# Optimization experiments

Hardware: AMD Instinct MI355X
Metric: run time of the kernel (lower is better)

## Reference

```python
import jax, jax.numpy as jnp
import numpy as np

B, N = 512, 500  # batch (cells), n_nodes (genes)


def setup_inputs() -> dict:
    key = jax.random.key(0)
    k1, k2, k3, k4 = jax.random.split(key, 4)
    x = jax.random.normal(k1, (B, N), dtype=jnp.float32)
    # GumbelAdjacency edge logits (bicycle initializes these near a constant; random here)
    log_alpha = jax.random.normal(k2, (N, N), dtype=jnp.float32)
    # single Linear(n_nodes, n_nodes, bias=False) weight, torch layout [out, in]
    W = jax.random.normal(k3, (N, N), dtype=jnp.float32) / np.sqrt(N).astype(np.float32)
    # uniform noise consumed by the gumbel-sigmoid sampler (one draw per batch element)
    u = jax.random.uniform(k4, (B, N, N), dtype=jnp.float32)
    return {"x": x, "log_alpha": log_alpha, "W": W, "u": u}


def reference(x, log_alpha, W, u):
    # --- GumbelAdjacency.forward(num_batch): hard gumbel-sigmoid sample, tau=1 ---
    eps = 1e-6
    uc = jnp.clip(u, eps, 1.0 - eps)
    logistic = jnp.log(uc) - jnp.log(1.0 - uc)            # logistic(0,1) noise
    y_soft = jax.nn.sigmoid(log_alpha[None, :, :] + logistic)  # [B, N, N]
    y_hard = (y_soft > 0.5).astype(y_soft.dtype)
    adj = y_soft + jax.lax.stop_gradient(y_hard - y_soft)  # straight-through

    # --- per-node masked MLP loop, fused ---
    # original: f_x[b, i] = tanh( (mask_i * adj[b, :, i] * x[b]) @ W.T )[i]
    #                     = tanh( sum_{j != i} W[i, j] * adj[b, j, i] * x[b, j] )
    mask = 1.0 - jnp.eye(N, dtype=x.dtype)                # mask[j, i] = 0 iff j == i
    gated = adj * mask[None, :, :]                        # [B, j, i]
    f_x = jnp.tanh(jnp.einsum('bji,bj,ij->bi', gated, x, W))  # [B, N]
    return f_x
```

## Files before the change

kernel.cpp:

```cpp
#include <hip/hip_runtime.h>
#include <math.h>

#define NN 500
#define BB 512
#define NCHUNK 4
#define JCH (NN / NCHUNK)

__device__ __forceinline__ bool np_decision(float laf, float v) {
    float l1 = (float)log((double)v);
    float s  = 1.0f - v;
    float l2 = (float)log((double)s);
    float logistic = l1 - l2;
    float z  = laf + logistic;
    float e  = (float)exp(-(double)z);
    float d  = 1.0f + e;
    float y  = 1.0f / d;
    return y > 0.5f;
}

__global__ void prep_kernel(const float* __restrict__ la,
                            const float* __restrict__ W,
                            float2* __restrict__ WU) {
    int idx = blockIdx.x * blockDim.x + threadIdx.x;
    if (idx >= NN * NN) return;
    int j = idx / NN;
    int i = idx - j * NN;
    float laf = la[idx];

    const float LO = 1e-6f;
    const float HI = (float)(1.0 - 1e-6);

    float U;
    if (!np_decision(laf, HI)) {
        U = __builtin_inff();
    } else if (np_decision(laf, LO)) {
        U = 0.0f;
    } else {
        unsigned lo = __float_as_uint(LO);
        unsigned hi = __float_as_uint(HI);
        double T  = 1.0 / (1.0 + exp((double)laf));
        float  Tf = fminf(fmaxf((float)T, LO), HI);
        unsigned g = __float_as_uint(Tf);
        unsigned a = (g > lo + 1024u) ? g - 1024u : lo;
        unsigned b = (g + 1024u < hi) ? g + 1024u : hi;
        if (!np_decision(laf, __uint_as_float(b))) {
            lo = b;
        } else {
            hi = b;
            if (np_decision(laf, __uint_as_float(a))) hi = a; else lo = a;
        }
        while (hi - lo > 1u) {
            unsigned mid = lo + (hi - lo) / 2u;
            if (np_decision(laf, __uint_as_float(mid))) hi = mid; else lo = mid;
        }
        U = __uint_as_float(hi);
    }
    float w = (i == j) ? 0.0f : W[i * NN + j];
    WU[idx] = make_float2(w, U);
}

__global__ __launch_bounds__(256) void fused_kernel(
        const float* __restrict__ x,
        const float* __restrict__ u,
        const float4* __restrict__ WU4,
        float* __restrict__ P) {
    __shared__ float xs[JCH];
    const int bid = blockIdx.x;
    const int b = bid >> 2;
    const int c = bid & 3;
    const int j0 = c * JCH;
    const int t = threadIdx.x;
    if (t < JCH) xs[t] = x[b * NN + j0 + t];
    __syncthreads();
    if (t >= NN / 2) return;

    const float2* __restrict__ u2 = (const float2*)(u + (size_t)b * NN * NN) + j0 * (NN / 2);
    const float4* __restrict__ wu = WU4 + j0 * (NN / 2);

    const float LO = 1e-6f;
    const float HI = (float)(1.0 - 1e-6);

    float acc0 = 0.0f, acc1 = 0.0f;
#pragma unroll 5
    for (int j = 0; j < JCH; ++j) {
        const int k = j * (NN / 2) + t;
        float2 uv = u2[k];
        float4 wv = wu[k];
        float  xj = xs[j];
        float uc0 = fminf(fmaxf(uv.x, LO), HI);
        float uc1 = fminf(fmaxf(uv.y, LO), HI);
        if (uc0 >= wv.y) acc0 += wv.x * xj;
        if (uc1 >= wv.w) acc1 += wv.z * xj;
    }
    float2 o = make_float2(acc0, acc1);
    ((float2*)(P + (size_t)c * BB * NN + b * NN))[t] = o;
}

__global__ __launch_bounds__(256) void reduce_kernel(const float* __restrict__ P,
                                                     float* __restrict__ out) {
    int n = blockIdx.x * blockDim.x + threadIdx.x;
    if (n >= BB * NN) return;
    const int S = BB * NN;
    float s = P[n] + P[S + n] + P[2 * S + n] + P[3 * S + n];
    out[n] = tanhf(s);
}

extern "C" void kernel_launch(void* const* d_in, const int* in_sizes, int n_in,
                              void* d_out, int out_size, void* d_ws, size_t ws_size,
                              hipStream_t stream) {
    const float* x  = (const float*)d_in[0];
    const float* la = (const float*)d_in[1];
    const float* W  = (const float*)d_in[2];
    const float* u  = (const float*)d_in[3];
    float* out = (float*)d_out;

    float2* WU = (float2*)d_ws;
    float*  P  = (float*)((char*)d_ws + (size_t)NN * NN * sizeof(float2));

    int prep_blocks = (NN * NN + 255) / 256;
    prep_kernel<<<prep_blocks, 256, 0, stream>>>(la, W, WU);
    fused_kernel<<<BB * NCHUNK, 256, 0, stream>>>(x, u, (const float4*)WU, P);
    reduce_kernel<<<(BB * NN + 255) / 256, 256, 0, stream>>>(P, out);
}
```

Before: 707.8 us.

## Share WU loads across four batch rows and use nontemporal u loads

The fused kernel now handles four batch elements per block, so each loaded WU entry (weight and threshold) serves four u rows instead of one. It also splits the j dimension into 10 chunks instead of 4, loads u with nontemporal hints, and drops the redundant clamp of u. The reduce kernel is vectorised to float4 and sums 10 partials, which makes the partial buffer larger. The prep bisection now starts with a narrower ±32-ulp bracket around the guess.

```diff
diff --git a/kernel.cpp b/kernel.cpp
--- a/kernel.cpp
+++ b/kernel.cpp
@@ -3,8 +3,12 @@
 
 #define NN 500
 #define BB 512
-#define NCHUNK 4
+#define BGRP 4
+#define NCHUNK 10
 #define JCH (NN / NCHUNK)
+#define NPAIR (NN / 2)
+
+using f2 = __attribute__((ext_vector_type(2))) float;
 
 __device__ __forceinline__ bool np_decision(float laf, float v) {
     float l1 = (float)log((double)v);
@@ -41,13 +45,13 @@
         double T  = 1.0 / (1.0 + exp((double)laf));
         float  Tf = fminf(fmaxf((float)T, LO), HI);
         unsigned g = __float_as_uint(Tf);
-        unsigned a = (g > lo + 1024u) ? g - 1024u : lo;
-        unsigned b = (g + 1024u < hi) ? g + 1024u : hi;
-        if (!np_decision(laf, __uint_as_float(b))) {
-            lo = b;
-        } else {
-            hi = b;
+        unsigned a = (g > lo + 32u) ? g - 32u : lo;
+        unsigned b = (g + 32u < hi) ? g + 32u : hi;
+        if (a > lo) {
             if (np_decision(laf, __uint_as_float(a))) hi = a; else lo = a;
+        }
+        if (b > lo && b < hi) {
+            if (np_decision(laf, __uint_as_float(b))) hi = b; else lo = b;
         }
         while (hi - lo > 1u) {
             unsigned mid = lo + (hi - lo) / 2u;
@@ -64,45 +68,65 @@
         const float* __restrict__ u,
         const float4* __restrict__ WU4,
         float* __restrict__ P) {
-    __shared__ float xs[JCH];
+    __shared__ float xs[BGRP][JCH];
     const int bid = blockIdx.x;
-    const int b = bid >> 2;
-    const int c = bid & 3;
+    const int bg = bid / NCHUNK;
+    const int c  = bid - bg * NCHUNK;
+    const int b0 = bg * BGRP;
     const int j0 = c * JCH;
     const int t = threadIdx.x;
-    if (t < JCH) xs[t] = x[b * NN + j0 + t];
+    if (t < BGRP * JCH) {
+        int bl = t / JCH;
+        int j  = t - bl * JCH;
+        xs[bl][j] = x[(b0 + bl) * NN + j0 + j];
+    }
     __syncthreads();
-    if (t >= NN / 2) return;
+    if (t >= NPAIR) return;
 
-    const float2* __restrict__ u2 = (const float2*)(u + (size_t)b * NN * NN) + j0 * (NN / 2);
-    const float4* __restrict__ wu = WU4 + j0 * (NN / 2);
+    const f2* __restrict__ u0 = (const f2*)(u + (size_t)(b0 + 0) * NN * NN);
+    const f2* __restrict__ u1 = (const f2*)(u + (size_t)(b0 + 1) * NN * NN);
+    const f2* __restrict__ u2 = (const f2*)(u + (size_t)(b0 + 2) * NN * NN);
+    const f2* __restrict__ u3 = (const f2*)(u + (size_t)(b0 + 3) * NN * NN);
 
-    const float LO = 1e-6f;
-    const float HI = (float)(1.0 - 1e-6);
-
-    float acc0 = 0.0f, acc1 = 0.0f;
+    float a00 = 0.0f, a01 = 0.0f, a10 = 0.0f, a11 = 0.0f;
+    float a20 = 0.0f, a21 = 0.0f, a30 = 0.0f, a31 = 0.0f;
+    int k = j0 * NPAIR + t;
 #pragma unroll 5
-    for (int j = 0; j < JCH; ++j) {
-        const int k = j * (NN / 2) + t;
-        float2 uv = u2[k];
-        float4 wv = wu[k];
-        float  xj = xs[j];
-        float uc0 = fminf(fmaxf(uv.x, LO), HI);
-        float uc1 = fminf(fmaxf(uv.y, LO), HI);
-        if (uc0 >= wv.y) acc0 += wv.x * xj;
-        if (uc1 >= wv.w) acc1 += wv.z * xj;
+    for (int j = 0; j < JCH; ++j, k += NPAIR) {
+        float4 wv = WU4[k];
+        f2 v0 = __builtin_nontemporal_load(u0 + k);
+        f2 v1 = __builtin_nontemporal_load(u1 + k);
+        f2 v2 = __builtin_nontemporal_load(u2 + k);
+        f2 v3 = __builtin_nontemporal_load(u3 + k);
+        float x0 = xs[0][j], x1 = xs[1][j], x2 = xs[2][j], x3 = xs[3][j];
+        if (v0.x >= wv.y) a00 += wv.x * x0;
+        if (v0.y >= wv.w) a01 += wv.z * x0;
+        if (v1.x >= wv.y) a10 += wv.x * x1;
+        if (v1.y >= wv.w) a11 += wv.z * x1;
+        if (v2.x >= wv.y) a20 += wv.x * x2;
+        if (v2.y >= wv.w) a21 += wv.z * x2;
+        if (v3.x >= wv.y) a30 += wv.x * x3;
+        if (v3.y >= wv.w) a31 += wv.z * x3;
     }
-    float2 o = make_float2(acc0, acc1);
-    ((float2*)(P + (size_t)c * BB * NN + b * NN))[t] = o;
+    float* Pb = P + ((size_t)c * BB + b0) * NN;
+    ((float2*)(Pb + 0 * NN))[t] = make_float2(a00, a01);
+    ((float2*)(Pb + 1 * NN))[t] = make_float2(a10, a11);
+    ((float2*)(Pb + 2 * NN))[t] = make_float2(a20, a21);
+    ((float2*)(Pb + 3 * NN))[t] = make_float2(a30, a31);
 }
 
 __global__ __launch_bounds__(256) void reduce_kernel(const float* __restrict__ P,
                                                      float* __restrict__ out) {
-    int n = blockIdx.x * blockDim.x + threadIdx.x;
-    if (n >= BB * NN) return;
+    int n4 = blockIdx.x * blockDim.x + threadIdx.x;
+    if (n4 >= BB * NN / 4) return;
     const int S = BB * NN;
-    float s = P[n] + P[S + n] + P[2 * S + n] + P[3 * S + n];
-    out[n] = tanhf(s);
+    float4 s = ((const float4*)P)[n4];
+#pragma unroll
+    for (int cc = 1; cc < NCHUNK; ++cc) {
+        float4 p = ((const float4*)(P + (size_t)cc * S))[n4];
+        s.x += p.x; s.y += p.y; s.z += p.z; s.w += p.w;
+    }
+    ((float4*)out)[n4] = make_float4(tanhf(s.x), tanhf(s.y), tanhf(s.z), tanhf(s.w));
 }
 
 extern "C" void kernel_launch(void* const* d_in, const int* in_sizes, int n_in,
@@ -119,6 +143,6 @@
 
     int prep_blocks = (NN * NN + 255) / 256;
     prep_kernel<<<prep_blocks, 256, 0, stream>>>(la, W, WU);
-    fused_kernel<<<BB * NCHUNK, 256, 0, stream>>>(x, u, (const float4*)WU, P);
-    reduce_kernel<<<(BB * NN + 255) / 256, 256, 0, stream>>>(P, out);
+    fused_kernel<<<(BB / BGRP) * NCHUNK, 256, 0, stream>>>(x, u, (const float4*)WU, P);
+    reduce_kernel<<<(BB * NN / 4 + 255) / 256, 256, 0, stream>>>(P, out);
 }
```

After: 669.1 us. 5.5% less time.

## Fuse partial-sum reduction into main kernel and restructure j/i work split

Applied to the files above, without the earlier changes.

Each block now covers one batch row and half the output columns across all j, with two thread groups splitting j and combining their partials in shared memory. This removes the separate reduce kernel and the partial-sum round trip through global memory. The u stream is read with nontemporal loads and the explicit clamp is dropped, which assumes the precomputed thresholds already absorb clamping. The prep bisection now starts from a tighter bracket around the initial guess, so it needs fewer decision evaluations.

```diff
diff --git a/kernel.cpp b/kernel.cpp
--- a/kernel.cpp
+++ b/kernel.cpp
@@ -3,8 +3,12 @@
 
 #define NN 500
 #define BB 512
-#define NCHUNK 4
-#define JCH (NN / NCHUNK)
+#define ISPL 2
+#define IPAIR (NN / 2)
+#define IBP (IPAIR / ISPL)
+#define JP 2
+
+using f2 = __attribute__((ext_vector_type(2))) float;
 
 __device__ __forceinline__ bool np_decision(float laf, float v) {
     float l1 = (float)log((double)v);
@@ -41,13 +45,13 @@
         double T  = 1.0 / (1.0 + exp((double)laf));
         float  Tf = fminf(fmaxf((float)T, LO), HI);
         unsigned g = __float_as_uint(Tf);
-        unsigned a = (g > lo + 1024u) ? g - 1024u : lo;
-        unsigned b = (g + 1024u < hi) ? g + 1024u : hi;
-        if (!np_decision(laf, __uint_as_float(b))) {
-            lo = b;
-        } else {
-            hi = b;
+        unsigned a = (g > lo + 8u) ? g - 8u : lo;
+        unsigned b = (g + 8u < hi) ? g + 8u : hi;
+        if (a > lo) {
             if (np_decision(laf, __uint_as_float(a))) hi = a; else lo = a;
+        }
+        if (b > lo && b < hi) {
+            if (np_decision(laf, __uint_as_float(b))) hi = b; else lo = b;
         }
         while (hi - lo > 1u) {
             unsigned mid = lo + (hi - lo) / 2u;
@@ -62,47 +66,44 @@
 __global__ __launch_bounds__(256) void fused_kernel(
         const float* __restrict__ x,
         const float* __restrict__ u,
-        const float4* __restrict__ WU4,
-        float* __restrict__ P) {
-    __shared__ float xs[JCH];
+        const float2* __restrict__ WU,
+        float* __restrict__ out) {
+    __shared__ float xs[NN];
+    __shared__ float2 red[128];
     const int bid = blockIdx.x;
-    const int b = bid >> 2;
-    const int c = bid & 3;
-    const int j0 = c * JCH;
-    const int t = threadIdx.x;
-    if (t < JCH) xs[t] = x[b * NN + j0 + t];
+    const int b   = bid >> 1;
+    const int ic  = bid & 1;
+    const int i0p = ic * IBP;
+    const int t  = threadIdx.x;
+    const int tj = t >> 7;
+    const int tp = t & 127;
+
+    for (int o = t; o < NN; o += 256) xs[o] = x[b * NN + o];
     __syncthreads();
-    if (t >= NN / 2) return;
 
-    const float2* __restrict__ u2 = (const float2*)(u + (size_t)b * NN * NN) + j0 * (NN / 2);
-    const float4* __restrict__ wu = WU4 + j0 * (NN / 2);
+    float a0 = 0.0f, a1 = 0.0f;
+    if (tp < IBP) {
+        const f2* __restrict__ up  = (const f2*)(u + (size_t)b * NN * NN);
+        const float4* __restrict__ wu4 = (const float4*)WU;
+        int k = tj * IPAIR + i0p + tp;
+#pragma unroll 10
+        for (int js = 0; js < NN / JP; ++js) {
+            f2     v  = __builtin_nontemporal_load(up + k);
+            float4 wv = wu4[k];
+            float  xj = xs[js * JP + tj];
+            if (v.x >= wv.y) a0 += wv.x * xj;
+            if (v.y >= wv.w) a1 += wv.z * xj;
+            k += JP * IPAIR;
+        }
+    }
 
-    const float LO = 1e-6f;
-    const float HI = (float)(1.0 - 1e-6);
-
-    float acc0 = 0.0f, acc1 = 0.0f;
-#pragma unroll 5
-    for (int j = 0; j < JCH; ++j) {
-        const int k = j * (NN / 2) + t;
-        float2 uv = u2[k];
-        float4 wv = wu[k];
-        float  xj = xs[j];
-        float uc0 = fminf(fmaxf(uv.x, LO), HI);
-        float uc1 = fminf(fmaxf(uv.y, LO), HI);
-        if (uc0 >= wv.y) acc0 += wv.x * xj;
-        if (uc1 >= wv.w) acc1 += wv.z * xj;
+    if (tj) red[tp] = make_float2(a0, a1);
+    __syncthreads();
+    if (!tj && tp < IBP) {
+        float2 r = red[tp];
+        float2 o = make_float2(tanhf(a0 + r.x), tanhf(a1 + r.y));
+        ((float2*)(out + b * NN + 2 * i0p))[tp] = o;
     }
-    float2 o = make_float2(acc0, acc1);
-    ((float2*)(P + (size_t)c * BB * NN + b * NN))[t] = o;
-}
-
-__global__ __launch_bounds__(256) void reduce_kernel(const float* __restrict__ P,
-                                                     float* __restrict__ out) {
-    int n = blockIdx.x * blockDim.x + threadIdx.x;
-    if (n >= BB * NN) return;
-    const int S = BB * NN;
-    float s = P[n] + P[S + n] + P[2 * S + n] + P[3 * S + n];
-    out[n] = tanhf(s);
 }
 
 extern "C" void kernel_launch(void* const* d_in, const int* in_sizes, int n_in,
@@ -115,10 +116,8 @@
     float* out = (float*)d_out;
 
     float2* WU = (float2*)d_ws;
-    float*  P  = (float*)((char*)d_ws + (size_t)NN * NN * sizeof(float2));
 
     int prep_blocks = (NN * NN + 255) / 256;
     prep_kernel<<<prep_blocks, 256, 0, stream>>>(la, W, WU);
-    fused_kernel<<<BB * NCHUNK, 256, 0, stream>>>(x, u, (const float4*)WU, P);
-    reduce_kernel<<<(BB * NN + 255) / 256, 256, 0, stream>>>(P, out);
+    fused_kernel<<<BB * ISPL, 256, 0, stream>>>(x, u, WU, out);
 }
```

Result: slower. 779.3 us (+10.1%).
